# Performance work log

Measured on AMD Instinct MI355X. Metric: run time of the kernel, lower is better.

Reference implementation:

```python
import jax, jax.numpy as jnp
import numpy as np

N = 100000      # nodes
E = 1600000     # edges (avg degree 16)
D_IN, D_H1, D_H2, D_OUT = 512, 256, 256, 64


def setup_inputs() -> dict:
    key = jax.random.key(0)
    ks = jax.random.split(key, 8)
    x = jax.random.normal(ks[0], (N, D_IN), dtype=jnp.float32)
    row = jax.random.randint(ks[1], (E,), 0, N, dtype=jnp.int32)
    col = jax.random.randint(ks[2], (E,), 0, N, dtype=jnp.int32)
    vals = jax.random.uniform(ks[3], (E,), dtype=jnp.float32)
    # xavier-normal-ish scaling for weights
    W1 = jax.random.normal(ks[4], (D_IN, D_H1), dtype=jnp.float32) * np.sqrt(2.0 / (D_IN + D_H1))
    W2 = jax.random.normal(ks[5], (D_H1, D_H2), dtype=jnp.float32) * np.sqrt(2.0 / (D_H1 + D_H2))
    W3 = jax.random.normal(ks[6], (D_H2, D_OUT), dtype=jnp.float32) * np.sqrt(2.0 / (D_H2 + D_OUT))
    b1 = jnp.zeros((D_H1,), dtype=jnp.float32)
    b2 = jnp.zeros((D_H2,), dtype=jnp.float32)
    b3 = jnp.zeros((D_OUT,), dtype=jnp.float32)
    return {"x": x, "row": row, "col": col, "vals": vals,
            "W1": W1, "b1": b1, "W2": W2, "b2": b2, "W3": W3, "b3": b3}


def reference(x, row, col, vals, W1, b1, W2, b2, W3, b3):
    n = x.shape[0]

    def spmm(h):
        # out[i] = sum_{e: row[e]==i} vals[e] * h[col[e]]  (COO spmm)
        return jax.ops.segment_sum(vals[:, None] * h[col], row, num_segments=n)

    # layer 1: linear -> spmm -> relu  (dropout p=0 -> identity)
    h = jax.nn.relu(spmm(x @ W1 + b1))
    # layer 2
    h = jax.nn.relu(spmm(h @ W2 + b2))
    # output layer: no activation, no dropout
    return spmm(h @ W3 + b3)
```

## Files before the change

kernel.cpp:

```cpp
#include <hip/hip_runtime.h>

typedef _Float16 f16;
typedef _Float16 f16x4 __attribute__((ext_vector_type(4)));
typedef _Float16 f16x8 __attribute__((ext_vector_type(8)));
typedef float f32x4 __attribute__((ext_vector_type(4)));

#define DEVI __device__ __forceinline__

static constexpr int CAP = 64;

DEVI void g2l16(const void* g, void* l) {
  __builtin_amdgcn_global_load_lds(
      (const __attribute__((address_space(1))) void*)g,
      (__attribute__((address_space(3))) void*)l, 16, 0, 0);
}

DEVI f16x8 cvt8(float4 a, float4 b) {
  f16x8 r;
  r[0] = (f16)a.x; r[1] = (f16)a.y; r[2] = (f16)a.z; r[3] = (f16)a.w;
  r[4] = (f16)b.x; r[5] = (f16)b.y; r[6] = (f16)b.z; r[7] = (f16)b.w;
  return r;
}

__global__ __launch_bounds__(256)
void prep_w(const float* __restrict__ W1, const float* __restrict__ W2,
            const float* __restrict__ W3, f16* __restrict__ WT1,
            f16* __restrict__ WT2, f16* __restrict__ WT3) {
  int t = blockIdx.x * 256 + threadIdx.x;
  if (t < 131072) {
    int n = t >> 9, k = t & 511;
    WT1[t] = (f16)W1[k * 256 + n];
  } else if (t < 131072 + 65536) {
    int u = t - 131072; int n = u >> 8, k = u & 255;
    WT2[u] = (f16)W2[k * 256 + n];
  } else if (t < 131072 + 65536 + 16384) {
    int u = t - 131072 - 65536; int n = u >> 8, k = u & 255;
    WT3[u] = (f16)W3[k * 64 + n];
  }
}

__global__ __launch_bounds__(256)
void build_slots(const int* __restrict__ row, const int* __restrict__ col,
                 const float* __restrict__ vals, int* __restrict__ cnt,
                 int2* __restrict__ slots, int E) {
  int e = blockIdx.x * 256 + threadIdx.x;
  if (e >= E) return;
  int r = row[e];
  int p = atomicAdd(&cnt[r], 1);
  if (p < CAP) slots[(size_t)r * CAP + p] = make_int2(col[e], __float_as_int(vals[e]));
}

template <int NT, int WN, int KI, bool AF32>
__global__ __launch_bounds__(256)
void gemm_lds(const void* __restrict__ Ap, const f16* __restrict__ WT,
              const float* __restrict__ bias, f16* __restrict__ C,
              int M, int N) {
  constexpr int K = KI * 32;
  constexpr int RPB = (4 / WN) * 32;
  constexpr int BN = WN * NT * 16;
  __shared__ alignas(16) char AsB[RPB * 32 * (AF32 ? 4 : 2)];
  __shared__ alignas(16) char BsB[BN * 32 * 2];

  const int tid = threadIdx.x;
  const int wave = tid >> 6, lane = tid & 63;
  const int quad = lane >> 4, l16 = lane & 15;
  const int wn = (WN == 1) ? 0 : (wave & 1);
  const int wm = (WN == 1) ? wave : (wave >> 1);
  const int r0 = blockIdx.x * RPB;

  f32x4 acc[2][NT];
#pragma unroll
  for (int mt = 0; mt < 2; ++mt)
#pragma unroll
    for (int nt = 0; nt < NT; ++nt) {
      f32x4 z = {0.f, 0.f, 0.f, 0.f};
      acc[mt][nt] = z;
    }

  for (int kb = 0; kb < KI; ++kb) {
    if constexpr (AF32) {
      const float* Af = (const float*)Ap;
      const int rowg = min(r0 + wave * 16 + l16, M - 1);
#pragma unroll
      for (int t = 0; t < 2; ++t) {
        const float* gp = Af + (size_t)rowg * K + kb * 32 + (t * 4 + quad) * 4;
        g2l16(gp, AsB + wave * 2048 + t * 1024);
      }
    } else {
      const f16* Ah = (const f16*)Ap;
#pragma unroll
      for (int t = 0; t < RPB / 64; ++t) {
        const int blk = wave * (RPB / 64) + t;
        const int rowg = min(r0 + blk * 16 + l16, M - 1);
        const f16* gp = Ah + (size_t)rowg * K + kb * 32 + quad * 8;
        g2l16(gp, AsB + blk * 1024);
      }
    }
#pragma unroll
    for (int t = 0; t < BN / 64; ++t) {
      const int blk = wave * (BN / 64) + t;
      const int n = blk * 16 + l16;
      const f16* gp = WT + (size_t)n * K + kb * 32 + quad * 8;
      g2l16(gp, BsB + blk * 1024);
    }
    __syncthreads();

    f16x8 af[2];
#pragma unroll
    for (int mt = 0; mt < 2; ++mt) {
      const int blk = wm * 2 + mt;
      if constexpr (AF32) {
        const float4* p = (const float4*)(AsB + blk * 2048);
        float4 a0 = p[quad * 32 + l16];
        float4 a1 = p[quad * 32 + 16 + l16];
        af[mt] = cvt8(a0, a1);
      } else {
        af[mt] = *(const f16x8*)(AsB + blk * 1024 + (quad * 16 + l16) * 16);
      }
    }
    f16x8 bf[NT];
#pragma unroll
    for (int nt = 0; nt < NT; ++nt) {
      const int blk = wn * NT + nt;
      bf[nt] = *(const f16x8*)(BsB + blk * 1024 + (quad * 16 + l16) * 16);
    }
#pragma unroll
    for (int mt = 0; mt < 2; ++mt)
#pragma unroll
      for (int nt = 0; nt < NT; ++nt)
        acc[mt][nt] = __builtin_amdgcn_mfma_f32_16x16x32_f16(af[mt], bf[nt], acc[mt][nt], 0, 0, 0);
    __syncthreads();
  }

  float bv[NT];
#pragma unroll
  for (int nt = 0; nt < NT; ++nt)
    bv[nt] = bias[wn * NT * 16 + nt * 16 + l16];
#pragma unroll
  for (int mt = 0; mt < 2; ++mt) {
#pragma unroll
    for (int nt = 0; nt < NT; ++nt) {
      const int colg = wn * NT * 16 + nt * 16 + l16;
#pragma unroll
      for (int r = 0; r < 4; ++r) {
        const int grow = r0 + wm * 32 + mt * 16 + quad * 4 + r;
        if (grow < M)
          C[(size_t)grow * N + colg] = (f16)(acc[mt][nt][r] + bv[nt]);
      }
    }
  }
}

__global__ __launch_bounds__(256)
void spmm_relu256(const f16* __restrict__ T, const int2* __restrict__ slots,
                  const int* __restrict__ cnt, f16* __restrict__ H, int nrows) {
  const int wave = threadIdx.x >> 6, lane = threadIdx.x & 63;
  const int i = blockIdx.x * 4 + wave;
  if (i >= nrows) return;
  const int c = min(cnt[i], CAP);
  const int2* sl = slots + (size_t)i * CAP;
  const int half = lane >> 5, fl = lane & 31;

  float a[8];
#pragma unroll
  for (int k = 0; k < 8; ++k) a[k] = 0.f;

  int j = 0;
  for (; j + 16 <= c; j += 16) {
    int2 e[8];
#pragma unroll
    for (int t = 0; t < 8; ++t) e[t] = sl[j + 2 * t + half];
    f16x8 u[8];
#pragma unroll
    for (int t = 0; t < 8; ++t)
      u[t] = *(const f16x8*)(T + (size_t)e[t].x * 256 + fl * 8);
#pragma unroll
    for (int t = 0; t < 8; ++t) {
      const float v = __int_as_float(e[t].y);
#pragma unroll
      for (int k = 0; k < 8; ++k) a[k] += v * (float)u[t][k];
    }
  }
  for (; j + 8 <= c; j += 8) {
    int2 e0 = sl[j + half], e1 = sl[j + 2 + half];
    int2 e2 = sl[j + 4 + half], e3 = sl[j + 6 + half];
    f16x8 u0 = *(const f16x8*)(T + (size_t)e0.x * 256 + fl * 8);
    f16x8 u1 = *(const f16x8*)(T + (size_t)e1.x * 256 + fl * 8);
    f16x8 u2 = *(const f16x8*)(T + (size_t)e2.x * 256 + fl * 8);
    f16x8 u3 = *(const f16x8*)(T + (size_t)e3.x * 256 + fl * 8);
    float v0 = __int_as_float(e0.y), v1 = __int_as_float(e1.y);
    float v2 = __int_as_float(e2.y), v3 = __int_as_float(e3.y);
#pragma unroll
    for (int k = 0; k < 8; ++k)
      a[k] += v0 * (float)u0[k] + v1 * (float)u1[k] + v2 * (float)u2[k] + v3 * (float)u3[k];
  }
  for (; j < c; j += 2) {
    const int jj = j + half;
    int2 e = sl[min(jj, c - 1)];
    const float v = (jj < c) ? __int_as_float(e.y) : 0.f;
    f16x8 u = *(const f16x8*)(T + (size_t)e.x * 256 + fl * 8);
#pragma unroll
    for (int k = 0; k < 8; ++k) a[k] += v * (float)u[k];
  }
#pragma unroll
  for (int k = 0; k < 8; ++k) a[k] += __shfl_xor(a[k], 32, 64);
  if (half == 0) {
    f16x8 o;
#pragma unroll
    for (int k = 0; k < 8; ++k) o[k] = (f16)fmaxf(a[k], 0.f);
    *(f16x8*)(H + (size_t)i * 256 + fl * 8) = o;
  }
}

__global__ __launch_bounds__(256)
void spmm_out64(const f16* __restrict__ T, const int2* __restrict__ slots,
                const int* __restrict__ cnt, float* __restrict__ out, int nrows) {
  const int wave = threadIdx.x >> 6, lane = threadIdx.x & 63;
  const int i = blockIdx.x * 4 + wave;
  if (i >= nrows) return;
  const int c = min(cnt[i], CAP);
  const int2* sl = slots + (size_t)i * CAP;
  const int sub = lane >> 4, fl = lane & 15;

  float a[4];
#pragma unroll
  for (int k = 0; k < 4; ++k) a[k] = 0.f;

  int j = 0;
  for (; j + 16 <= c; j += 16) {
    int2 e[4];
#pragma unroll
    for (int t = 0; t < 4; ++t) e[t] = sl[j + 4 * t + sub];
    f16x4 u[4];
#pragma unroll
    for (int t = 0; t < 4; ++t)
      u[t] = *(const f16x4*)(T + (size_t)e[t].x * 64 + fl * 4);
#pragma unroll
    for (int t = 0; t < 4; ++t) {
      const float v = __int_as_float(e[t].y);
#pragma unroll
      for (int k = 0; k < 4; ++k) a[k] += v * (float)u[t][k];
    }
  }
  for (; j < c; j += 4) {
    const int jj = j + sub;
    int2 e = sl[min(jj, c - 1)];
    const float v = (jj < c) ? __int_as_float(e.y) : 0.f;
    f16x4 u = *(const f16x4*)(T + (size_t)e.x * 64 + fl * 4);
#pragma unroll
    for (int k = 0; k < 4; ++k) a[k] += v * (float)u[k];
  }
#pragma unroll
  for (int k = 0; k < 4; ++k) {
    a[k] += __shfl_xor(a[k], 16, 64);
    a[k] += __shfl_xor(a[k], 32, 64);
  }
  if (sub == 0) {
    float4 o = make_float4(a[0], a[1], a[2], a[3]);
    *(float4*)(out + (size_t)i * 64 + fl * 4) = o;
  }
}

extern "C" void kernel_launch(void* const* d_in, const int* in_sizes, int n_in,
                              void* d_out, int out_size, void* d_ws, size_t ws_size,
                              hipStream_t stream) {
  const float* x    = (const float*)d_in[0];
  const int*   row  = (const int*)d_in[1];
  const int*   col  = (const int*)d_in[2];
  const float* vals = (const float*)d_in[3];
  const float* W1   = (const float*)d_in[4];
  const float* b1   = (const float*)d_in[5];
  const float* W2   = (const float*)d_in[6];
  const float* b2   = (const float*)d_in[7];
  const float* W3   = (const float*)d_in[8];
  const float* b3   = (const float*)d_in[9];
  float* out = (float*)d_out;

  const int N = in_sizes[0] / 512;
  const int E = in_sizes[1];

  char* ws = (char*)d_ws;
  const size_t MiB = 1ull << 20;
  int*  cnt   = (int*)ws;
  int2* slots = (int2*)(ws + 1 * MiB);
  f16*  WT1   = (f16*)(ws + 52 * MiB);
  f16*  WT2   = WT1 + 256 * 512;
  f16*  WT3   = WT2 + 256 * 256;
  f16*  T     = (f16*)(ws + 53 * MiB);
  f16*  H     = (f16*)(ws + 104 * MiB);

  hipMemsetAsync(cnt, 0, (size_t)N * sizeof(int), stream);
  prep_w<<<(131072 + 65536 + 16384 + 255) / 256, 256, 0, stream>>>(W1, W2, W3, WT1, WT2, WT3);
  build_slots<<<(E + 255) / 256, 256, 0, stream>>>(row, col, vals, cnt, slots, E);

  const int g12 = (N + 63) / 64;
  const int g3  = (N + 127) / 128;
  const int gs  = (N + 3) / 4;

  gemm_lds<8, 2, 16, true><<<g12, 256, 0, stream>>>(x, WT1, b1, T, N, 256);
  spmm_relu256<<<gs, 256, 0, stream>>>(T, slots, cnt, H, N);
  gemm_lds<8, 2, 8, false><<<g12, 256, 0, stream>>>(H, WT2, b2, T, N, 256);
  spmm_relu256<<<gs, 256, 0, stream>>>(T, slots, cnt, H, N);
  gemm_lds<4, 1, 8, false><<<g3, 256, 0, stream>>>(H, WT3, b3, T, N, 64);
  spmm_out64<<<gs, 256, 0, stream>>>(T, slots, cnt, out, N);
}
```

Before: 831.8 us.

## Pre-tile activations and weights into MFMA fragment layout, drop LDS from GEMMs

```diff
diff --git a/kernel.cpp b/kernel.cpp
--- a/kernel.cpp
+++ b/kernel.cpp
@@ -22,20 +22,44 @@
   return r;
 }
 
-__global__ __launch_bounds__(256)
-void prep_w(const float* __restrict__ W1, const float* __restrict__ W2,
-            const float* __restrict__ W3, f16* __restrict__ WT1,
-            f16* __restrict__ WT2, f16* __restrict__ WT3) {
-  int t = blockIdx.x * 256 + threadIdx.x;
-  if (t < 131072) {
-    int n = t >> 9, k = t & 511;
-    WT1[t] = (f16)W1[k * 256 + n];
-  } else if (t < 131072 + 65536) {
-    int u = t - 131072; int n = u >> 8, k = u & 255;
-    WT2[u] = (f16)W2[k * 256 + n];
-  } else if (t < 131072 + 65536 + 16384) {
-    int u = t - 131072 - 65536; int n = u >> 8, k = u & 255;
-    WT3[u] = (f16)W3[k * 64 + n];
+
+template <int N_, int KIm, int L2KI>
+__global__ __launch_bounds__(256)
+void prep_w_t(const float* __restrict__ W, f16* __restrict__ out, int total) {
+  int o = blockIdx.x * 256 + threadIdx.x;
+  if (o >= total) return;
+  int j = o & 7, l16 = (o >> 3) & 15, quad = (o >> 7) & 3;
+  int rest = o >> 9;
+  int kb = rest & (KIm - 1);
+  int ntile = rest >> L2KI;
+  int n = ntile * 16 + l16, k = kb * 32 + quad * 8 + j;
+  out[o] = (f16)W[k * N_ + n];
+}
+
+__global__ __launch_bounds__(256)
+void convert_x(const float* __restrict__ x, f16* __restrict__ xt) {
+  __shared__ float Xs[16 * 516];
+  const int tile = blockIdx.x;
+  const int tid = threadIdx.x;
+  const int wave = tid >> 6, lane = tid & 63;
+#pragma unroll
+  for (int it = 0; it < 4; ++it) {
+    const int r = wave * 4 + it;
+    const float* src = x + ((size_t)tile * 16 + r) * 512 + lane * 4;
+#pragma unroll
+    for (int h = 0; h < 2; ++h)
+      g2l16(src + h * 256, &Xs[r * 516 + h * 256]);
+  }
+  __syncthreads();
+#pragma unroll
+  for (int i = 0; i < 4; ++i) {
+    const int s = i * 256 + tid;
+    const int kb = s >> 6, ln = s & 63;
+    const int row = ln & 15, k8 = kb * 32 + ((ln >> 4) << 3);
+    float4 a = *(const float4*)&Xs[row * 516 + k8];
+    float4 b = *(const float4*)&Xs[row * 516 + k8 + 4];
+    f16x8 v = cvt8(a, b);
+    *(f16x8*)((char*)xt + ((size_t)tile * 16 + kb) * 1024 + ln * 16) = v;
   }
 }
 
@@ -50,23 +74,18 @@
   if (p < CAP) slots[(size_t)r * CAP + p] = make_int2(col[e], __float_as_int(vals[e]));
 }
 
-template <int NT, int WN, int KI, bool AF32>
-__global__ __launch_bounds__(256)
-void gemm_lds(const void* __restrict__ Ap, const f16* __restrict__ WT,
-              const float* __restrict__ bias, f16* __restrict__ C,
-              int M, int N) {
-  constexpr int K = KI * 32;
-  constexpr int RPB = (4 / WN) * 32;
-  constexpr int BN = WN * NT * 16;
-  __shared__ alignas(16) char AsB[RPB * 32 * (AF32 ? 4 : 2)];
-  __shared__ alignas(16) char BsB[BN * 32 * 2];
-
+template <int KI, int NT, int WN>
+__global__ __launch_bounds__(256, 3)
+void gemm_t(const f16* __restrict__ At, const f16* __restrict__ Bt,
+            const float* __restrict__ bias, f16* __restrict__ C,
+            int M, int Ncols, int Atiles) {
   const int tid = threadIdx.x;
   const int wave = tid >> 6, lane = tid & 63;
   const int quad = lane >> 4, l16 = lane & 15;
-  const int wn = (WN == 1) ? 0 : (wave & 1);
-  const int wm = (WN == 1) ? wave : (wave >> 1);
-  const int r0 = blockIdx.x * RPB;
+  const int wn = (WN == 2) ? (wave & 1) : 0;
+  const int wm = (WN == 2) ? (wave >> 1) : wave;
+  const int r0 = blockIdx.x * ((4 / WN) * 32) + wm * 32;
+  const int n0 = wn * NT * 16;
 
   f32x4 acc[2][NT];
 #pragma unroll
@@ -77,138 +96,118 @@
       acc[mt][nt] = z;
     }
 
+  const int t0 = min(r0 >> 4, Atiles - 1);
+  const int t1 = min((r0 >> 4) + 1, Atiles - 1);
+  const f16* a0p = At + (size_t)t0 * KI * 512 + lane * 8;
+  const f16* a1p = At + (size_t)t1 * KI * 512 + lane * 8;
+  const f16* bp  = Bt + (size_t)(wn * NT) * KI * 512 + lane * 8;
+
+#pragma unroll 2
   for (int kb = 0; kb < KI; ++kb) {
-    if constexpr (AF32) {
-      const float* Af = (const float*)Ap;
-      const int rowg = min(r0 + wave * 16 + l16, M - 1);
-#pragma unroll
-      for (int t = 0; t < 2; ++t) {
-        const float* gp = Af + (size_t)rowg * K + kb * 32 + (t * 4 + quad) * 4;
-        g2l16(gp, AsB + wave * 2048 + t * 1024);
+    f16x8 af0 = *(const f16x8*)(a0p + kb * 512);
+    f16x8 af1 = *(const f16x8*)(a1p + kb * 512);
+    f16x8 bf[NT];
+#pragma unroll
+    for (int nt = 0; nt < NT; ++nt)
+      bf[nt] = *(const f16x8*)(bp + ((size_t)nt * KI + kb) * 512);
+#pragma unroll
+    for (int nt = 0; nt < NT; ++nt) {
+      acc[0][nt] = __builtin_amdgcn_mfma_f32_16x16x32_f16(af0, bf[nt], acc[0][nt], 0, 0, 0);
+      acc[1][nt] = __builtin_amdgcn_mfma_f32_16x16x32_f16(af1, bf[nt], acc[1][nt], 0, 0, 0);
+    }
+  }
+
+  float bv[NT];
+#pragma unroll
+  for (int nt = 0; nt < NT; ++nt)
+    bv[nt] = bias[n0 + nt * 16 + l16];
+#pragma unroll
+  for (int mt = 0; mt < 2; ++mt) {
+#pragma unroll
+    for (int nt = 0; nt < NT; ++nt) {
+      const int colg = n0 + nt * 16 + l16;
+#pragma unroll
+      for (int r = 0; r < 4; ++r) {
+        const int grow = r0 + mt * 16 + quad * 4 + r;
+        if (grow < M)
+          C[(size_t)grow * Ncols + colg] = (f16)(acc[mt][nt][r] + bv[nt]);
       }
-    } else {
-      const f16* Ah = (const f16*)Ap;
-#pragma unroll
-      for (int t = 0; t < RPB / 64; ++t) {
-        const int blk = wave * (RPB / 64) + t;
-        const int rowg = min(r0 + blk * 16 + l16, M - 1);
-        const f16* gp = Ah + (size_t)rowg * K + kb * 32 + quad * 8;
-        g2l16(gp, AsB + blk * 1024);
+    }
+  }
+}
+
+__global__ __launch_bounds__(256)
+void spmm_relu256_t(const f16* __restrict__ T, const int2* __restrict__ slots,
+                    const int* __restrict__ cnt, f16* __restrict__ Ht) {
+  __shared__ f16 Hs[16 * 280];
+  const int tid = threadIdx.x;
+  const int wave = tid >> 6, lane = tid & 63;
+  const int half = lane >> 5, fl = lane & 31;
+  const int base = blockIdx.x * 16;
+
+#pragma unroll 1
+  for (int it = 0; it < 4; ++it) {
+    const int i = base + wave * 4 + it;
+    const int c = min(cnt[i], CAP);
+    const int2* sl = slots + (size_t)i * CAP;
+    float a[8];
+#pragma unroll
+    for (int k = 0; k < 8; ++k) a[k] = 0.f;
+
+    int j = 0;
+    for (; j + 16 <= c; j += 16) {
+      int2 e[8];
+#pragma unroll
+      for (int t = 0; t < 8; ++t) e[t] = sl[j + 2 * t + half];
+      f16x8 u[8];
+#pragma unroll
+      for (int t = 0; t < 8; ++t)
+        u[t] = *(const f16x8*)(T + (size_t)e[t].x * 256 + fl * 8);
+#pragma unroll
+      for (int t = 0; t < 8; ++t) {
+        const float v = __int_as_float(e[t].y);
+#pragma unroll
+        for (int k = 0; k < 8; ++k) a[k] += v * (float)u[t][k];
       }
     }
-#pragma unroll
-    for (int t = 0; t < BN / 64; ++t) {
-      const int blk = wave * (BN / 64) + t;
-      const int n = blk * 16 + l16;
-      const f16* gp = WT + (size_t)n * K + kb * 32 + quad * 8;
-      g2l16(gp, BsB + blk * 1024);
-    }
-    __syncthreads();
-
-    f16x8 af[2];
-#pragma unroll
-    for (int mt = 0; mt < 2; ++mt) {
-      const int blk = wm * 2 + mt;
-      if constexpr (AF32) {
-        const float4* p = (const float4*)(AsB + blk * 2048);
-        float4 a0 = p[quad * 32 + l16];
-        float4 a1 = p[quad * 32 + 16 + l16];
-        af[mt] = cvt8(a0, a1);
-      } else {
-        af[mt] = *(const f16x8*)(AsB + blk * 1024 + (quad * 16 + l16) * 16);
-      }
-    }
-    f16x8 bf[NT];
-#pragma unroll
-    for (int nt = 0; nt < NT; ++nt) {
-      const int blk = wn * NT + nt;
-      bf[nt] = *(const f16x8*)(BsB + blk * 1024 + (quad * 16 + l16) * 16);
-    }
-#pragma unroll
-    for (int mt = 0; mt < 2; ++mt)
-#pragma unroll
-      for (int nt = 0; nt < NT; ++nt)
-        acc[mt][nt] = __builtin_amdgcn_mfma_f32_16x16x32_f16(af[mt], bf[nt], acc[mt][nt], 0, 0, 0);
-    __syncthreads();
-  }
-
-  float bv[NT];
-#pragma unroll
-  for (int nt = 0; nt < NT; ++nt)
-    bv[nt] = bias[wn * NT * 16 + nt * 16 + l16];
-#pragma unroll
-  for (int mt = 0; mt < 2; ++mt) {
-#pragma unroll
-    for (int nt = 0; nt < NT; ++nt) {
-      const int colg = wn * NT * 16 + nt * 16 + l16;
-#pragma unroll
-      for (int r = 0; r < 4; ++r) {
-        const int grow = r0 + wm * 32 + mt * 16 + quad * 4 + r;
-        if (grow < M)
-          C[(size_t)grow * N + colg] = (f16)(acc[mt][nt][r] + bv[nt]);
-      }
-    }
-  }
-}
-
-__global__ __launch_bounds__(256)
-void spmm_relu256(const f16* __restrict__ T, const int2* __restrict__ slots,
-                  const int* __restrict__ cnt, f16* __restrict__ H, int nrows) {
-  const int wave = threadIdx.x >> 6, lane = threadIdx.x & 63;
-  const int i = blockIdx.x * 4 + wave;
-  if (i >= nrows) return;
-  const int c = min(cnt[i], CAP);
-  const int2* sl = slots + (size_t)i * CAP;
-  const int half = lane >> 5, fl = lane & 31;
-
-  float a[8];
-#pragma unroll
-  for (int k = 0; k < 8; ++k) a[k] = 0.f;
-
-  int j = 0;
-  for (; j + 16 <= c; j += 16) {
-    int2 e[8];
-#pragma unroll
-    for (int t = 0; t < 8; ++t) e[t] = sl[j + 2 * t + half];
-    f16x8 u[8];
-#pragma unroll
-    for (int t = 0; t < 8; ++t)
-      u[t] = *(const f16x8*)(T + (size_t)e[t].x * 256 + fl * 8);
-#pragma unroll
-    for (int t = 0; t < 8; ++t) {
-      const float v = __int_as_float(e[t].y);
-#pragma unroll
-      for (int k = 0; k < 8; ++k) a[k] += v * (float)u[t][k];
-    }
-  }
-  for (; j + 8 <= c; j += 8) {
-    int2 e0 = sl[j + half], e1 = sl[j + 2 + half];
-    int2 e2 = sl[j + 4 + half], e3 = sl[j + 6 + half];
-    f16x8 u0 = *(const f16x8*)(T + (size_t)e0.x * 256 + fl * 8);
-    f16x8 u1 = *(const f16x8*)(T + (size_t)e1.x * 256 + fl * 8);
-    f16x8 u2 = *(const f16x8*)(T + (size_t)e2.x * 256 + fl * 8);
-    f16x8 u3 = *(const f16x8*)(T + (size_t)e3.x * 256 + fl * 8);
-    float v0 = __int_as_float(e0.y), v1 = __int_as_float(e1.y);
-    float v2 = __int_as_float(e2.y), v3 = __int_as_float(e3.y);
-#pragma unroll
-    for (int k = 0; k < 8; ++k)
-      a[k] += v0 * (float)u0[k] + v1 * (float)u1[k] + v2 * (float)u2[k] + v3 * (float)u3[k];
-  }
-  for (; j < c; j += 2) {
-    const int jj = j + half;
-    int2 e = sl[min(jj, c - 1)];
-    const float v = (jj < c) ? __int_as_float(e.y) : 0.f;
-    f16x8 u = *(const f16x8*)(T + (size_t)e.x * 256 + fl * 8);
-#pragma unroll
-    for (int k = 0; k < 8; ++k) a[k] += v * (float)u[k];
-  }
-#pragma unroll
-  for (int k = 0; k < 8; ++k) a[k] += __shfl_xor(a[k], 32, 64);
-  if (half == 0) {
-    f16x8 o;
-#pragma unroll
-    for (int k = 0; k < 8; ++k) o[k] = (f16)fmaxf(a[k], 0.f);
-    *(f16x8*)(H + (size_t)i * 256 + fl * 8) = o;
+    for (; j + 8 <= c; j += 8) {
+      int2 e0 = sl[j + half], e1 = sl[j + 2 + half];
+      int2 e2 = sl[j + 4 + half], e3 = sl[j + 6 + half];
+      f16x8 u0 = *(const f16x8*)(T + (size_t)e0.x * 256 + fl * 8);
+      f16x8 u1 = *(const f16x8*)(T + (size_t)e1.x * 256 + fl * 8);
+      f16x8 u2 = *(const f16x8*)(T + (size_t)e2.x * 256 + fl * 8);
+      f16x8 u3 = *(const f16x8*)(T + (size_t)e3.x * 256 + fl * 8);
+      float v0 = __int_as_float(e0.y), v1 = __int_as_float(e1.y);
+      float v2 = __int_as_float(e2.y), v3 = __int_as_float(e3.y);
+#pragma unroll
+      for (int k = 0; k < 8; ++k)
+        a[k] += v0 * (float)u0[k] + v1 * (float)u1[k] + v2 * (float)u2[k] + v3 * (float)u3[k];
+    }
+    for (; j < c; j += 2) {
+      const int jj = j + half;
+      int2 e = sl[min(jj, c - 1)];
+      const float v = (jj < c) ? __int_as_float(e.y) : 0.f;
+      f16x8 u = *(const f16x8*)(T + (size_t)e.x * 256 + fl * 8);
+#pragma unroll
+      for (int k = 0; k < 8; ++k) a[k] += v * (float)u[k];
+    }
+#pragma unroll
+    for (int k = 0; k < 8; ++k) a[k] += __shfl_xor(a[k], 32, 64);
+    if (half == 0) {
+      f16x8 o;
+#pragma unroll
+      for (int k = 0; k < 8; ++k) o[k] = (f16)fmaxf(a[k], 0.f);
+      *(f16x8*)&Hs[(wave * 4 + it) * 280 + fl * 8] = o;
+    }
+  }
+  __syncthreads();
+#pragma unroll
+  for (int i2 = 0; i2 < 2; ++i2) {
+    const int s = i2 * 256 + tid;
+    const int kb = s >> 6, ln = s & 63;
+    const int row = ln & 15, k8 = kb * 32 + ((ln >> 4) << 3);
+    f16x8 v = *(const f16x8*)&Hs[row * 280 + k8];
+    *(f16x8*)((char*)Ht + ((size_t)blockIdx.x * 8 + kb) * 1024 + ln * 16) = v;
   }
 }
 
@@ -278,29 +277,35 @@
 
   const int N = in_sizes[0] / 512;
   const int E = in_sizes[1];
+  const int NTILES = N / 16;
 
   char* ws = (char*)d_ws;
-  const size_t MiB = 1ull << 20;
-  int*  cnt   = (int*)ws;
-  int2* slots = (int2*)(ws + 1 * MiB);
-  f16*  WT1   = (f16*)(ws + 52 * MiB);
-  f16*  WT2   = WT1 + 256 * 512;
-  f16*  WT3   = WT2 + 256 * 256;
-  f16*  T     = (f16*)(ws + 53 * MiB);
-  f16*  H     = (f16*)(ws + 104 * MiB);
+  const size_t offB = 102432768;
+  const size_t offC = offB + 51200000;
+  f16*  xt    = (f16*)ws;
+  int2* slots = (int2*)ws;
+  f16*  Ht    = (f16*)(ws + 51200000);
+  f16*  T     = (f16*)(ws + offB);
+  f16*  T3    = (f16*)(ws + offB);
+  int*  cnt   = (int*)(ws + offC);
+  f16*  W1t   = (f16*)(ws + offC + 400000);
+  f16*  W2t   = W1t + 131072;
+  f16*  W3t   = W2t + 65536;
 
   hipMemsetAsync(cnt, 0, (size_t)N * sizeof(int), stream);
-  prep_w<<<(131072 + 65536 + 16384 + 255) / 256, 256, 0, stream>>>(W1, W2, W3, WT1, WT2, WT3);
-  build_slots<<<(E + 255) / 256, 256, 0, stream>>>(row, col, vals, cnt, slots, E);
+  prep_w_t<256, 16, 4><<<(131072 + 255) / 256, 256, 0, stream>>>(W1, W1t, 131072);
+  prep_w_t<256, 8, 3><<<(65536 + 255) / 256, 256, 0, stream>>>(W2, W2t, 65536);
+  prep_w_t<64, 8, 3><<<(16384 + 255) / 256, 256, 0, stream>>>(W3, W3t, 16384);
+  convert_x<<<NTILES, 256, 0, stream>>>(x, xt);
 
   const int g12 = (N + 63) / 64;
   const int g3  = (N + 127) / 128;
-  const int gs  = (N + 3) / 4;
-
-  gemm_lds<8, 2, 16, true><<<g12, 256, 0, stream>>>(x, WT1, b1, T, N, 256);
-  spmm_relu256<<<gs, 256, 0, stream>>>(T, slots, cnt, H, N);
-  gemm_lds<8, 2, 8, false><<<g12, 256, 0, stream>>>(H, WT2, b2, T, N, 256);
-  spmm_relu256<<<gs, 256, 0, stream>>>(T, slots, cnt, H, N);
-  gemm_lds<4, 1, 8, false><<<g3, 256, 0, stream>>>(H, WT3, b3, T, N, 64);
-  spmm_out64<<<gs, 256, 0, stream>>>(T, slots, cnt, out, N);
-}
+
+  gemm_t<16, 8, 2><<<g12, 256, 0, stream>>>(xt, W1t, b1, T, N, 256, NTILES);
+  build_slots<<<(E + 255) / 256, 256, 0, stream>>>(row, col, vals, cnt, slots, E);
+  spmm_relu256_t<<<NTILES, 256, 0, stream>>>(T, slots, cnt, Ht);
+  gemm_t<8, 8, 2><<<g12, 256, 0, stream>>>(Ht, W2t, b2, T, N, 256, NTILES);
+  spmm_relu256_t<<<NTILES, 256, 0, stream>>>(T, slots, cnt, Ht);
+  gemm_t<8, 4, 1><<<g3, 256, 0, stream>>>(Ht, W3t, b3, T3, N, 64, NTILES);
+  spmm_out64<<<(N + 3) / 4, 256, 0, stream>>>(T3, slots, cnt, out, N);
+}
```

New measurement: 888.5 us. 1.07x slower.
